# Performance work log

Measured on AMD Instinct MI355X. Metric: run time of the kernel, lower is better.

## Reference

```python
import jax, jax.numpy as jnp
import numpy as np

TIME_SHIFT_START = 256
VELOCITY_START = 768
NOTE_OFF_START = 128
RHYTHM_W = 1.0
HARMONY_W = 1.0
MELODY_W = 1.0


def setup_inputs() -> dict:
    key = jax.random.key(0)
    tokens = jax.random.randint(key, (512, 16384), 0, 774, dtype=jnp.int64)
    return {"tokens": tokens}


def reference(tokens) -> jnp.ndarray:
    batch_size, seq_len = tokens.shape

    # --- rhythm consistency: |diff| of time-shift indicator, mean over all ---
    time_shifts = ((tokens >= TIME_SHIFT_START) & (tokens < VELOCITY_START)).astype(jnp.float32)
    rhythm_loss = jnp.abs(jnp.diff(time_shifts, axis=1)).mean()

    # --- harmonic coherence: vectorized version of the per-position loop ---
    # original: sum_i mean_b(harsh[:, i]) / seq_len  ==  harsh.sum() / (batch * seq_len)
    note_on_mask = tokens < NOTE_OFF_START
    pitches = tokens * note_on_mask.astype(tokens.dtype)
    pitch_classes = pitches % 12                      # [B, S]
    interval = jnp.abs(pitch_classes[:, :-1] - pitch_classes[:, 1:])  # [B, S-1]
    harsh = ((interval == 6) | (interval == 11)).astype(jnp.float32)
    harmony_loss = harsh.sum() / (batch_size * seq_len)

    # --- melodic smoothness: large leap (>12 semitones) rate ---
    pitch_diffs = jnp.diff(pitches.astype(jnp.float32), axis=1)
    melody_loss = (jnp.abs(pitch_diffs) > 12).astype(jnp.float32).mean()

    return RHYTHM_W * rhythm_loss + HARMONY_W * harmony_loss + MELODY_W * melody_loss
```

## Files before the change

### kernel.cpp

```cpp
#include <hip/hip_runtime.h>

constexpr int B = 512;
constexpr int S = 16384;
constexpr int NTOK = B * S;
constexpr int TPT = 16;
constexpr int NBLOCKS = NTOK / TPT / 256;

__global__ __launch_bounds__(256) void mpl_main(const int* __restrict__ tokens,
                                                unsigned int* __restrict__ partials) {
    const int tid = blockIdx.x * 256 + threadIdx.x;
    const int t0 = tid * TPT;

    int toks[TPT + 1];
    const int4* p = reinterpret_cast<const int4*>(tokens + t0);
    int4 x0 = p[0], x1 = p[1], x2 = p[2], x3 = p[3];
    toks[0]  = x0.x; toks[1]  = x0.y; toks[2]  = x0.z; toks[3]  = x0.w;
    toks[4]  = x1.x; toks[5]  = x1.y; toks[6]  = x1.z; toks[7]  = x1.w;
    toks[8]  = x2.x; toks[9]  = x2.y; toks[10] = x2.z; toks[11] = x2.w;
    toks[12] = x3.x; toks[13] = x3.y; toks[14] = x3.z; toks[15] = x3.w;

    const int rowEnd = ((t0 + TPT) & (S - 1)) == 0 ? 0 : 1;
    toks[TPT] = tokens[t0 + 15 + rowEnd];

    int rc = 0, hc = 0, mc = 0;
    int qp = 0, pcp = 0, pitp = 0;
#pragma unroll
    for (int j = 0; j <= TPT; ++j) {
        const int t = toks[j];
        const int q = (t + 256) >> 9;
        const int pit = (t < 128) ? t : 0;
        const int pc = pit % 12;
        if (j > 0) {
            rc += (qp ^ q) & 1;
            const int xh = pcp - pc + 11;
            hc += (0x00420021u >> xh) & 1;
            const unsigned ym = (unsigned)(pitp - pit + 12);
            mc += (ym > 24u) ? 1 : 0;
        }
        qp = q; pcp = pc; pitp = pit;
    }

    unsigned int pk = (unsigned)rc | ((unsigned)mc << 16);
    unsigned int hh = (unsigned)hc;
#pragma unroll
    for (int off = 32; off > 0; off >>= 1) {
        pk += __shfl_down(pk, off, 64);
        hh += __shfl_down(hh, off, 64);
    }

    __shared__ unsigned int s[2][4];
    const int wave = threadIdx.x >> 6;
    if ((threadIdx.x & 63) == 0) {
        s[0][wave] = pk;
        s[1][wave] = hh;
    }
    __syncthreads();
    if (threadIdx.x == 0) {
        unsigned int pks = s[0][0] + s[0][1] + s[0][2] + s[0][3];
        unsigned int hs  = s[1][0] + s[1][1] + s[1][2] + s[1][3];
        partials[0 * NBLOCKS + blockIdx.x] = pks & 0xFFFFu;
        partials[1 * NBLOCKS + blockIdx.x] = hs;
        partials[2 * NBLOCKS + blockIdx.x] = pks >> 16;
    }
}

__global__ __launch_bounds__(256) void mpl_reduce(const unsigned int* __restrict__ partials,
                                                  float* __restrict__ out) {
    unsigned int c0 = 0, c1 = 0, c2 = 0;
    for (int j = threadIdx.x; j < NBLOCKS; j += 256) {
        c0 += partials[0 * NBLOCKS + j];
        c1 += partials[1 * NBLOCKS + j];
        c2 += partials[2 * NBLOCKS + j];
    }
#pragma unroll
    for (int off = 32; off > 0; off >>= 1) {
        c0 += __shfl_down(c0, off, 64);
        c1 += __shfl_down(c1, off, 64);
        c2 += __shfl_down(c2, off, 64);
    }
    __shared__ unsigned int s[3][4];
    const int wave = threadIdx.x >> 6;
    if ((threadIdx.x & 63) == 0) {
        s[0][wave] = c0; s[1][wave] = c1; s[2][wave] = c2;
    }
    __syncthreads();
    if (threadIdx.x == 0) {
        unsigned int r = s[0][0] + s[0][1] + s[0][2] + s[0][3];
        unsigned int h = s[1][0] + s[1][1] + s[1][2] + s[1][3];
        unsigned int m = s[2][0] + s[2][1] + s[2][2] + s[2][3];
        const double pairs = (double)B * (double)(S - 1);
        const double all = (double)B * (double)S;
        out[0] = (float)((double)r / pairs + (double)h / all + (double)m / pairs);
    }
}

extern "C" void kernel_launch(void* const* d_in, const int* in_sizes, int n_in,
                              void* d_out, int out_size, void* d_ws, size_t ws_size,
                              hipStream_t stream) {
    const int* tokens = (const int*)d_in[0];
    unsigned int* partials = (unsigned int*)d_ws;

    mpl_main<<<NBLOCKS, 256, 0, stream>>>(tokens, partials);
    mpl_reduce<<<1, 256, 0, stream>>>(partials, (float*)d_out);
}
```

Before: 16.40 us.

## Fuse final reduction into main kernel via atomics and last-block ticket

Replaces the separate reduce kernel with per-block atomic accumulation into 32 spread cache lines, with a ticket counter so the last block finalizes the output. It removes the second kernel and the partials round-trip through memory. In exchange it adds a memset of the workspace on every call, plus atomics and a threadfence at the end of each block.

```diff
diff --git a/kernel.cpp b/kernel.cpp
--- a/kernel.cpp
+++ b/kernel.cpp
@@ -5,9 +5,12 @@
 constexpr int NTOK = B * S;
 constexpr int TPT = 16;
 constexpr int NBLOCKS = NTOK / TPT / 256;
+constexpr int NLINES = 32;
+constexpr int WS_ZERO_BYTES = NLINES * 64 + 64;
 
-__global__ __launch_bounds__(256) void mpl_main(const int* __restrict__ tokens,
-                                                unsigned int* __restrict__ partials) {
+__global__ __launch_bounds__(256) void mpl_fused(const int* __restrict__ tokens,
+                                                 unsigned int* __restrict__ ws,
+                                                 float* __restrict__ out) {
     const int tid = blockIdx.x * 256 + threadIdx.x;
     const int t0 = tid * TPT;
 
@@ -49,48 +52,49 @@
     }
 
     __shared__ unsigned int s[2][4];
+    __shared__ unsigned int sLast;
     const int wave = threadIdx.x >> 6;
     if ((threadIdx.x & 63) == 0) {
         s[0][wave] = pk;
         s[1][wave] = hh;
     }
     __syncthreads();
+
+    unsigned int* acc = ws;
+    unsigned int* ticket = ws + NLINES * 16;
+
     if (threadIdx.x == 0) {
         unsigned int pks = s[0][0] + s[0][1] + s[0][2] + s[0][3];
         unsigned int hs  = s[1][0] + s[1][1] + s[1][2] + s[1][3];
-        partials[0 * NBLOCKS + blockIdx.x] = pks & 0xFFFFu;
-        partials[1 * NBLOCKS + blockIdx.x] = hs;
-        partials[2 * NBLOCKS + blockIdx.x] = pks >> 16;
-    }
-}
-
-__global__ __launch_bounds__(256) void mpl_reduce(const unsigned int* __restrict__ partials,
-                                                  float* __restrict__ out) {
-    unsigned int c0 = 0, c1 = 0, c2 = 0;
-    for (int j = threadIdx.x; j < NBLOCKS; j += 256) {
-        c0 += partials[0 * NBLOCKS + j];
-        c1 += partials[1 * NBLOCKS + j];
-        c2 += partials[2 * NBLOCKS + j];
-    }
-#pragma unroll
-    for (int off = 32; off > 0; off >>= 1) {
-        c0 += __shfl_down(c0, off, 64);
-        c1 += __shfl_down(c1, off, 64);
-        c2 += __shfl_down(c2, off, 64);
-    }
-    __shared__ unsigned int s[3][4];
-    const int wave = threadIdx.x >> 6;
-    if ((threadIdx.x & 63) == 0) {
-        s[0][wave] = c0; s[1][wave] = c1; s[2][wave] = c2;
+        const int line = (blockIdx.x & (NLINES - 1)) * 16;
+        atomicAdd(&acc[line + 0], pks & 0xFFFFu);
+        atomicAdd(&acc[line + 1], hs);
+        atomicAdd(&acc[line + 2], pks >> 16);
+        __threadfence();
+        unsigned int old = atomicAdd(ticket, 1u);
+        sLast = (old == (unsigned)(NBLOCKS - 1)) ? 1u : 0u;
     }
     __syncthreads();
-    if (threadIdx.x == 0) {
-        unsigned int r = s[0][0] + s[0][1] + s[0][2] + s[0][3];
-        unsigned int h = s[1][0] + s[1][1] + s[1][2] + s[1][3];
-        unsigned int m = s[2][0] + s[2][1] + s[2][2] + s[2][3];
-        const double pairs = (double)B * (double)(S - 1);
-        const double all = (double)B * (double)S;
-        out[0] = (float)((double)r / pairs + (double)h / all + (double)m / pairs);
+
+    if (sLast && threadIdx.x < 64) {
+        unsigned int r = 0, h = 0, m = 0;
+        if (threadIdx.x < NLINES) {
+            const int line = threadIdx.x * 16;
+            r = atomicAdd(&acc[line + 0], 0u);
+            h = atomicAdd(&acc[line + 1], 0u);
+            m = atomicAdd(&acc[line + 2], 0u);
+        }
+#pragma unroll
+        for (int off = 16; off > 0; off >>= 1) {
+            r += __shfl_down(r, off, 64);
+            h += __shfl_down(h, off, 64);
+            m += __shfl_down(m, off, 64);
+        }
+        if (threadIdx.x == 0) {
+            const double pairs = (double)B * (double)(S - 1);
+            const double all = (double)B * (double)S;
+            out[0] = (float)((double)r / pairs + (double)h / all + (double)m / pairs);
+        }
     }
 }
 
@@ -98,8 +102,8 @@
                               void* d_out, int out_size, void* d_ws, size_t ws_size,
                               hipStream_t stream) {
     const int* tokens = (const int*)d_in[0];
-    unsigned int* partials = (unsigned int*)d_ws;
+    unsigned int* ws = (unsigned int*)d_ws;
 
-    mpl_main<<<NBLOCKS, 256, 0, stream>>>(tokens, partials);
-    mpl_reduce<<<1, 256, 0, stream>>>(partials, (float*)d_out);
+    hipMemsetAsync(ws, 0, WS_ZERO_BYTES, stream);
+    mpl_fused<<<NBLOCKS, 256, 0, stream>>>(tokens, ws, (float*)d_out);
 }
```

New measurement: 51.11 us. 3.12x slower.

## Double tokens per thread, share boundary token via wave shuffle, pack partials

Applied to the files above, without the earlier changes.

Each thread now processes 32 tokens with eight int4 loads instead of 16 with four, which halves the number of blocks. The neighbour token is taken from the next lane by a cross-lane shuffle, so only the last lane of each wave issues a scalar global load. Partials are stored as two packed arrays instead of three, and the reduce kernel reads them with uint4 loads. The risk is higher register pressure and fewer waves in flight to hide load latency on a kernel that is bandwidth bound.

```diff
diff --git a/kernel.cpp b/kernel.cpp
--- a/kernel.cpp
+++ b/kernel.cpp
@@ -3,24 +3,32 @@
 constexpr int B = 512;
 constexpr int S = 16384;
 constexpr int NTOK = B * S;
-constexpr int TPT = 16;
+constexpr int TPT = 32;
 constexpr int NBLOCKS = NTOK / TPT / 256;
 
 __global__ __launch_bounds__(256) void mpl_main(const int* __restrict__ tokens,
                                                 unsigned int* __restrict__ partials) {
     const int tid = blockIdx.x * 256 + threadIdx.x;
+    const int lane = threadIdx.x & 63;
     const int t0 = tid * TPT;
 
     int toks[TPT + 1];
     const int4* p = reinterpret_cast<const int4*>(tokens + t0);
-    int4 x0 = p[0], x1 = p[1], x2 = p[2], x3 = p[3];
-    toks[0]  = x0.x; toks[1]  = x0.y; toks[2]  = x0.z; toks[3]  = x0.w;
-    toks[4]  = x1.x; toks[5]  = x1.y; toks[6]  = x1.z; toks[7]  = x1.w;
-    toks[8]  = x2.x; toks[9]  = x2.y; toks[10] = x2.z; toks[11] = x2.w;
-    toks[12] = x3.x; toks[13] = x3.y; toks[14] = x3.z; toks[15] = x3.w;
+#pragma unroll
+    for (int v = 0; v < TPT / 4; ++v) {
+        int4 x = p[v];
+        toks[v * 4 + 0] = x.x;
+        toks[v * 4 + 1] = x.y;
+        toks[v * 4 + 2] = x.z;
+        toks[v * 4 + 3] = x.w;
+    }
 
-    const int rowEnd = ((t0 + TPT) & (S - 1)) == 0 ? 0 : 1;
-    toks[TPT] = tokens[t0 + 15 + rowEnd];
+    int nxt = __shfl(toks[0], lane + 1, 64);
+    if (lane == 63) {
+        const bool rowEnd = ((t0 + TPT) & (S - 1)) == 0;
+        nxt = rowEnd ? toks[TPT - 1] : tokens[t0 + TPT];
+    }
+    toks[TPT] = nxt;
 
     int rc = 0, hc = 0, mc = 0;
     int qp = 0, pcp = 0, pitp = 0;
@@ -56,41 +64,43 @@
     }
     __syncthreads();
     if (threadIdx.x == 0) {
-        unsigned int pks = s[0][0] + s[0][1] + s[0][2] + s[0][3];
-        unsigned int hs  = s[1][0] + s[1][1] + s[1][2] + s[1][3];
-        partials[0 * NBLOCKS + blockIdx.x] = pks & 0xFFFFu;
-        partials[1 * NBLOCKS + blockIdx.x] = hs;
-        partials[2 * NBLOCKS + blockIdx.x] = pks >> 16;
+        partials[blockIdx.x]           = s[0][0] + s[0][1] + s[0][2] + s[0][3];
+        partials[NBLOCKS + blockIdx.x] = s[1][0] + s[1][1] + s[1][2] + s[1][3];
     }
 }
 
 __global__ __launch_bounds__(256) void mpl_reduce(const unsigned int* __restrict__ partials,
                                                   float* __restrict__ out) {
-    unsigned int c0 = 0, c1 = 0, c2 = 0;
-    for (int j = threadIdx.x; j < NBLOCKS; j += 256) {
-        c0 += partials[0 * NBLOCKS + j];
-        c1 += partials[1 * NBLOCKS + j];
-        c2 += partials[2 * NBLOCKS + j];
+    const uint4* ppk = reinterpret_cast<const uint4*>(partials);
+    const uint4* phh = reinterpret_cast<const uint4*>(partials + NBLOCKS);
+    unsigned int r = 0, m = 0, h = 0;
+#pragma unroll 1
+    for (int j = threadIdx.x; j < NBLOCKS / 4; j += 256) {
+        uint4 a = ppk[j];
+        r += (a.x & 0xFFFFu) + (a.y & 0xFFFFu) + (a.z & 0xFFFFu) + (a.w & 0xFFFFu);
+        m += (a.x >> 16) + (a.y >> 16) + (a.z >> 16) + (a.w >> 16);
+        uint4 b = phh[j];
+        h += b.x + b.y + b.z + b.w;
     }
 #pragma unroll
     for (int off = 32; off > 0; off >>= 1) {
-        c0 += __shfl_down(c0, off, 64);
-        c1 += __shfl_down(c1, off, 64);
-        c2 += __shfl_down(c2, off, 64);
+        r += __shfl_down(r, off, 64);
+        m += __shfl_down(m, off, 64);
+        h += __shfl_down(h, off, 64);
     }
     __shared__ unsigned int s[3][4];
     const int wave = threadIdx.x >> 6;
     if ((threadIdx.x & 63) == 0) {
-        s[0][wave] = c0; s[1][wave] = c1; s[2][wave] = c2;
+        s[0][wave] = r; s[1][wave] = m; s[2][wave] = h;
     }
     __syncthreads();
     if (threadIdx.x == 0) {
-        unsigned int r = s[0][0] + s[0][1] + s[0][2] + s[0][3];
-        unsigned int h = s[1][0] + s[1][1] + s[1][2] + s[1][3];
-        unsigned int m = s[2][0] + s[2][1] + s[2][2] + s[2][3];
+        unsigned int rt = s[0][0] + s[0][1] + s[0][2] + s[0][3];
+        unsigned int mt = s[1][0] + s[1][1] + s[1][2] + s[1][3];
+        unsigned int ht = s[2][0] + s[2][1] + s[2][2] + s[2][3];
         const double pairs = (double)B * (double)(S - 1);
         const double all = (double)B * (double)S;
-        out[0] = (float)((double)r / pairs + (double)h / all + (double)m / pairs);
+        out[0] = (float)((double)rt / pairs + (double)ht / all + (double)mt / pairs);
     }
 }
 
```

After: 15.83 us. 1.04x faster.
